# Performance work log

Measured on AMD Instinct MI355X. Metric: run time of the kernel, lower is better.

Reference implementation:

```python
import jax, jax.numpy as jnp
import numpy as np

B, T, C = 4, 2048, 1024
H = 16
D = C // H  # head_size = 64


def setup_inputs() -> dict:
    key = jax.random.key(0)
    k1, k2 = jax.random.split(key)
    x = jax.random.normal(k1, (B, T, C), dtype=jnp.float32)
    w_attn = jax.random.normal(k2, (C, 3 * C), dtype=jnp.float32) * (C ** -0.5)
    return {"x": x, "w_attn": w_attn}


def reference(x, w_attn):
    Bx, Tx, Cx = x.shape
    qkv = x @ w_attn                      # [B,T,3C] (no bias)
    q, k, v = jnp.split(qkv, 3, axis=-1)  # each [B,T,C]
    # [B,T,C] -> [B,H,T,D]
    q = q.reshape(Bx, Tx, H, D).transpose(0, 2, 1, 3)
    k = k.reshape(Bx, Tx, H, D).transpose(0, 2, 1, 3)
    v = v.reshape(Bx, Tx, H, D).transpose(0, 2, 1, 3)
    wei = jnp.einsum('bhqd,bhkd->bhqk', q, k) * (D ** -0.5)  # [B,H,T,T]
    causal = jnp.tril(jnp.ones((Tx, Tx), dtype=bool))
    wei = jnp.where(causal, wei, -jnp.inf)
    wei = jax.nn.softmax(wei, axis=-1)
    out = jnp.einsum('bhqk,bhkd->bhqd', wei, v)  # [B,H,T,D]
    out = out.transpose(0, 2, 1, 3).reshape(Bx, Tx, Cx)
    return out
```

## Files before the change

### kernel.cpp

```cpp
#include <hip/hip_runtime.h>
#include <hip/hip_bf16.h>

typedef __attribute__((ext_vector_type(8))) short bf16x8;
typedef __attribute__((ext_vector_type(4))) float f32x4;

#define T_SZ 2048
#define C_SZ 1024
#define H_SZ 16
#define D_SZ 64
#define N_SZ 3072
#define M_SZ 8192

__device__ __forceinline__ unsigned short f2bf(float f) {
    unsigned int u = __float_as_uint(f);
    unsigned int r = (u + 0x7fffu + ((u >> 16) & 1u)) >> 16;
    return (unsigned short)r;
}

__device__ __forceinline__ void gload_lds16(const void* g, void* l) {
    __builtin_amdgcn_global_load_lds(
        (const __attribute__((address_space(1))) unsigned int*)g,
        (__attribute__((address_space(3))) unsigned int*)l, 16, 0, 0);
}

__global__ __launch_bounds__(256) void k_convert(const float* __restrict__ in,
                                                 unsigned short* __restrict__ out, int n4) {
    int i = blockIdx.x * 256 + threadIdx.x;
    if (i >= n4) return;
    float4 v = ((const float4*)in)[i];
    ushort4 u;
    u.x = f2bf(v.x); u.y = f2bf(v.y); u.z = f2bf(v.z); u.w = f2bf(v.w);
    ((ushort4*)out)[i] = u;
}

__global__ __launch_bounds__(256) void k_transpose(const float* __restrict__ w,
                                                   unsigned short* __restrict__ wt) {
    __shared__ float tile[32][33];
    const int nb = blockIdx.x * 32;
    const int kb = blockIdx.y * 32;
    const int tx = threadIdx.x & 31;
    const int ty = threadIdx.x >> 5;
#pragma unroll
    for (int i = 0; i < 32; i += 8)
        tile[ty + i][tx] = w[(size_t)(kb + ty + i) * N_SZ + nb + tx];
    __syncthreads();
#pragma unroll
    for (int i = 0; i < 32; i += 8)
        wt[(size_t)(nb + ty + i) * C_SZ + kb + tx] = f2bf(tile[tx][ty + i]);
}

__global__ __launch_bounds__(256) void k_qkv_gemm(const unsigned short* __restrict__ A,
                                                  const unsigned short* __restrict__ Bt,
                                                  unsigned short* __restrict__ Qb,
                                                  unsigned short* __restrict__ Kb,
                                                  unsigned short* __restrict__ Vb) {
    __shared__ __align__(16) unsigned short As[128 * 32];
    __shared__ __align__(16) unsigned short Bs[128 * 32];
    const int tid = threadIdx.x;
    const int lane = tid & 63, wid = tid >> 6;
    const int wm = wid & 1, wn = wid >> 1;
    const int row0 = blockIdx.x * 128;
    const int col0 = blockIdx.y * 128;
    f32x4 acc[4][4] = {};
    const int c0 = 2 * wid, c1 = 2 * wid + 1;
    const int lr = lane >> 2, lk = (lane & 3) * 8;
    const int l15 = lane & 15, lg = lane >> 4;

    for (int kt = 0; kt < 1024; kt += 32) {
        __syncthreads();
        gload_lds16(A + (size_t)(row0 + c0 * 16 + lr) * 1024 + kt + lk, As + c0 * 512);
        gload_lds16(A + (size_t)(row0 + c1 * 16 + lr) * 1024 + kt + lk, As + c1 * 512);
        gload_lds16(Bt + (size_t)(col0 + c0 * 16 + lr) * 1024 + kt + lk, Bs + c0 * 512);
        gload_lds16(Bt + (size_t)(col0 + c1 * 16 + lr) * 1024 + kt + lk, Bs + c1 * 512);
        __syncthreads();
        bf16x8 af[4], bfr[4];
#pragma unroll
        for (int m = 0; m < 4; ++m)
            af[m] = *(const bf16x8*)&As[(wm * 64 + m * 16 + l15) * 32 + lg * 8];
#pragma unroll
        for (int n = 0; n < 4; ++n)
            bfr[n] = *(const bf16x8*)&Bs[(wn * 64 + n * 16 + l15) * 32 + lg * 8];
#pragma unroll
        for (int m = 0; m < 4; ++m)
#pragma unroll
            for (int n = 0; n < 4; ++n)
                acc[m][n] = __builtin_amdgcn_mfma_f32_16x16x32_bf16(af[m], bfr[n], acc[m][n], 0, 0, 0);
    }

    const int sel = col0 >> 10;
    unsigned short* dst = (sel == 0) ? Qb : ((sel == 1) ? Kb : Vb);
#pragma unroll
    for (int m = 0; m < 4; ++m) {
#pragma unroll
        for (int n = 0; n < 4; ++n) {
            int col = col0 + wn * 64 + n * 16 + l15;
            int cc = col & 1023;
            int h = cc >> 6, d = cc & 63;
#pragma unroll
            for (int i = 0; i < 4; ++i) {
                int row = row0 + wm * 64 + m * 16 + lg * 4 + i;
                int b = row >> 11, t = row & 2047;
                size_t idx = ((size_t)(b * 16 + h) * 2048 + t) * 64 + d;
                dst[idx] = f2bf(acc[m][n][i]);
            }
        }
    }
}

__global__ __launch_bounds__(256) void k_attn(const unsigned short* __restrict__ Qb,
                                              const unsigned short* __restrict__ Kb,
                                              const unsigned short* __restrict__ Vb,
                                              float* __restrict__ out) {
    const int qt = blockIdx.x;
    const int bh = blockIdx.y;
    const int bb = bh >> 4, hh = bh & 15;
    const unsigned short* Qp = Qb + (size_t)bh * T_SZ * D_SZ;
    const unsigned short* Kp = Kb + (size_t)bh * T_SZ * D_SZ;
    const unsigned short* Vp = Vb + (size_t)bh * T_SZ * D_SZ;
    const int tid = threadIdx.x, lane = tid & 63, wid = tid >> 6;
    const int l15 = lane & 15, lg = lane >> 4;
    const int q0 = qt * 64 + wid * 16;

    __shared__ __align__(16) unsigned short Vt[64][72];
    __shared__ __align__(16) unsigned short Pl[4][16][72];

    bf16x8 qf[2];
#pragma unroll
    for (int kh = 0; kh < 2; ++kh)
        qf[kh] = *(const bf16x8*)&Qp[(size_t)(q0 + l15) * 64 + kh * 32 + lg * 8];

    f32x4 oacc[4] = {};
    float mrow[4] = {-1e30f, -1e30f, -1e30f, -1e30f};
    float lrow[4] = {0.f, 0.f, 0.f, 0.f};
    const float scale = 0.125f;

    for (int kb = 0; kb <= qt; ++kb) {
        const int k0 = kb * 64;
        __syncthreads();
        {
            const int key = tid >> 2, dc = (tid & 3) * 16;
            bf16x8 v0 = *(const bf16x8*)&Vp[(size_t)(k0 + key) * 64 + dc];
            bf16x8 v1 = *(const bf16x8*)&Vp[(size_t)(k0 + key) * 64 + dc + 8];
#pragma unroll
            for (int j = 0; j < 8; ++j) {
                Vt[dc + j][key]     = (unsigned short)v0[j];
                Vt[dc + 8 + j][key] = (unsigned short)v1[j];
            }
        }
        __syncthreads();

        f32x4 s[4] = {};
#pragma unroll
        for (int ct = 0; ct < 4; ++ct) {
#pragma unroll
            for (int kh = 0; kh < 2; ++kh) {
                bf16x8 kf = *(const bf16x8*)&Kp[(size_t)(k0 + ct * 16 + l15) * 64 + kh * 32 + lg * 8];
                s[ct] = __builtin_amdgcn_mfma_f32_16x16x32_bf16(qf[kh], kf, s[ct], 0, 0, 0);
            }
        }
        if (kb == qt) {
#pragma unroll
            for (int ct = 0; ct < 4; ++ct) {
                int key = k0 + ct * 16 + l15;
#pragma unroll
                for (int i = 0; i < 4; ++i) {
                    int qrow = q0 + lg * 4 + i;
                    s[ct][i] = (key <= qrow) ? s[ct][i] * scale : -1e30f;
                }
            }
        } else {
#pragma unroll
            for (int ct = 0; ct < 4; ++ct)
#pragma unroll
                for (int i = 0; i < 4; ++i) s[ct][i] *= scale;
        }
        float p[4][4];
#pragma unroll
        for (int i = 0; i < 4; ++i) {
            float rmax = fmaxf(fmaxf(s[0][i], s[1][i]), fmaxf(s[2][i], s[3][i]));
            rmax = fmaxf(rmax, __shfl_xor(rmax, 1));
            rmax = fmaxf(rmax, __shfl_xor(rmax, 2));
            rmax = fmaxf(rmax, __shfl_xor(rmax, 4));
            rmax = fmaxf(rmax, __shfl_xor(rmax, 8));
            float mnew = fmaxf(mrow[i], rmax);
            float sc = __expf(mrow[i] - mnew);
            float rsum = 0.f;
#pragma unroll
            for (int ct = 0; ct < 4; ++ct) {
                float pv = __expf(s[ct][i] - mnew);
                p[ct][i] = pv;
                rsum += pv;
            }
            rsum += __shfl_xor(rsum, 1);
            rsum += __shfl_xor(rsum, 2);
            rsum += __shfl_xor(rsum, 4);
            rsum += __shfl_xor(rsum, 8);
            lrow[i] = lrow[i] * sc + rsum;
            mrow[i] = mnew;
#pragma unroll
            for (int ct = 0; ct < 4; ++ct) oacc[ct][i] *= sc;
        }
#pragma unroll
        for (int ct = 0; ct < 4; ++ct)
#pragma unroll
            for (int i = 0; i < 4; ++i)
                Pl[wid][lg * 4 + i][ct * 16 + l15] = f2bf(p[ct][i]);
#pragma unroll
        for (int ct = 0; ct < 4; ++ct) {
#pragma unroll
            for (int kh = 0; kh < 2; ++kh) {
                bf16x8 pf = *(const bf16x8*)&Pl[wid][l15][kh * 32 + lg * 8];
                bf16x8 vf = *(const bf16x8*)&Vt[ct * 16 + l15][kh * 32 + lg * 8];
                oacc[ct] = __builtin_amdgcn_mfma_f32_16x16x32_bf16(pf, vf, oacc[ct], 0, 0, 0);
            }
        }
    }
#pragma unroll
    for (int ct = 0; ct < 4; ++ct) {
#pragma unroll
        for (int i = 0; i < 4; ++i) {
            int qrow = q0 + lg * 4 + i;
            float val = oacc[ct][i] / lrow[i];
            out[((size_t)bb * T_SZ + qrow) * C_SZ + hh * 64 + ct * 16 + l15] = val;
        }
    }
}

extern "C" void kernel_launch(void* const* d_in, const int* in_sizes, int n_in,
                              void* d_out, int out_size, void* d_ws, size_t ws_size,
                              hipStream_t stream) {
    const float* x = (const float*)d_in[0];
    const float* w = (const float*)d_in[1];
    float* out = (float*)d_out;
    char* ws = (char*)d_ws;
    unsigned short* xb  = (unsigned short*)(ws);
    unsigned short* wtb = (unsigned short*)(ws + 16777216);
    unsigned short* Qb  = (unsigned short*)(ws + 16777216 + 6291456);
    unsigned short* Kb  = (unsigned short*)(ws + 16777216 + 6291456 + 16777216);
    unsigned short* Vb  = (unsigned short*)(ws + 16777216 + 6291456 + 2 * 16777216);

    k_convert<<<8192, 256, 0, stream>>>(x, xb, 2097152);
    k_transpose<<<dim3(96, 32), 256, 0, stream>>>(w, wtb);
    k_qkv_gemm<<<dim3(64, 24), 256, 0, stream>>>(xb, wtb, Qb, Kb, Vb);
    k_attn<<<dim3(32, 64), 256, 0, stream>>>(Qb, Kb, Vb, out);
}
```

Baseline: 388.0 us.

## Store V transposed from GEMM and restructure attention into 128-row register-fed blocks

The QKV GEMM epilogue now writes V in a transposed [b,h,d,t] layout using vectorised 4-element stores. The attention kernel therefore loads V fragments directly from global memory, removing the per-iteration LDS transpose and both block barriers. Each wave now handles two 16-row groups, so every query block covers 128 rows. K fragments are prefetched in registers for the next key tile, and the heaviest causal blocks are launched first. The cost is more register pressure and half as many blocks, which may lower occupancy.

```diff
diff --git a/kernel.cpp b/kernel.cpp
--- a/kernel.cpp
+++ b/kernel.cpp
@@ -53,7 +53,7 @@
                                                   const unsigned short* __restrict__ Bt,
                                                   unsigned short* __restrict__ Qb,
                                                   unsigned short* __restrict__ Kb,
-                                                  unsigned short* __restrict__ Vb) {
+                                                  unsigned short* __restrict__ Vtb) {
     __shared__ __align__(16) unsigned short As[128 * 32];
     __shared__ __align__(16) unsigned short Bs[128 * 32];
     const int tid = threadIdx.x;
@@ -88,141 +88,193 @@
     }
 
     const int sel = col0 >> 10;
-    unsigned short* dst = (sel == 0) ? Qb : ((sel == 1) ? Kb : Vb);
-#pragma unroll
-    for (int m = 0; m < 4; ++m) {
-#pragma unroll
-        for (int n = 0; n < 4; ++n) {
-            int col = col0 + wn * 64 + n * 16 + l15;
-            int cc = col & 1023;
-            int h = cc >> 6, d = cc & 63;
-#pragma unroll
-            for (int i = 0; i < 4; ++i) {
-                int row = row0 + wm * 64 + m * 16 + lg * 4 + i;
+    if (sel < 2) {
+        unsigned short* dst = (sel == 0) ? Qb : Kb;
+#pragma unroll
+        for (int m = 0; m < 4; ++m) {
+#pragma unroll
+            for (int n = 0; n < 4; ++n) {
+                int col = col0 + wn * 64 + n * 16 + l15;
+                int cc = col & 1023;
+                int h = cc >> 6, d = cc & 63;
+#pragma unroll
+                for (int i = 0; i < 4; ++i) {
+                    int row = row0 + wm * 64 + m * 16 + lg * 4 + i;
+                    int b = row >> 11, t = row & 2047;
+                    size_t idx = ((size_t)(b * 16 + h) * 2048 + t) * 64 + d;
+                    dst[idx] = f2bf(acc[m][n][i]);
+                }
+            }
+        }
+    } else {
+#pragma unroll
+        for (int m = 0; m < 4; ++m) {
+#pragma unroll
+            for (int n = 0; n < 4; ++n) {
+                int cc = (col0 + wn * 64 + n * 16 + l15) & 1023;
+                int h = cc >> 6, d = cc & 63;
+                int row = row0 + wm * 64 + m * 16 + lg * 4;
                 int b = row >> 11, t = row & 2047;
-                size_t idx = ((size_t)(b * 16 + h) * 2048 + t) * 64 + d;
-                dst[idx] = f2bf(acc[m][n][i]);
-            }
-        }
-    }
+                ushort4 u;
+                u.x = f2bf(acc[m][n][0]); u.y = f2bf(acc[m][n][1]);
+                u.z = f2bf(acc[m][n][2]); u.w = f2bf(acc[m][n][3]);
+                size_t idx = ((size_t)(b * 16 + h) * 64 + d) * 2048 + t;
+                *(ushort4*)&Vtb[idx] = u;
+            }
+        }
+    }
+}
+
+__device__ __forceinline__ void load_k(const unsigned short* __restrict__ Kp, int k0,
+                                       int l15, int lg, bf16x8 kf[4][2]) {
+#pragma unroll
+    for (int ct = 0; ct < 4; ++ct)
+#pragma unroll
+        for (int kh = 0; kh < 2; ++kh)
+            kf[ct][kh] = *(const bf16x8*)&Kp[(size_t)(k0 + ct * 16 + l15) * 64 + kh * 32 + lg * 8];
 }
 
 __global__ __launch_bounds__(256) void k_attn(const unsigned short* __restrict__ Qb,
                                               const unsigned short* __restrict__ Kb,
-                                              const unsigned short* __restrict__ Vb,
+                                              const unsigned short* __restrict__ Vt,
                                               float* __restrict__ out) {
-    const int qt = blockIdx.x;
+    const int qb = 15 - blockIdx.x;
     const int bh = blockIdx.y;
     const int bb = bh >> 4, hh = bh & 15;
     const unsigned short* Qp = Qb + (size_t)bh * T_SZ * D_SZ;
     const unsigned short* Kp = Kb + (size_t)bh * T_SZ * D_SZ;
-    const unsigned short* Vp = Vb + (size_t)bh * T_SZ * D_SZ;
+    const unsigned short* Vp = Vt + (size_t)bh * T_SZ * D_SZ;
     const int tid = threadIdx.x, lane = tid & 63, wid = tid >> 6;
     const int l15 = lane & 15, lg = lane >> 4;
-    const int q0 = qt * 64 + wid * 16;
-
-    __shared__ __align__(16) unsigned short Vt[64][72];
-    __shared__ __align__(16) unsigned short Pl[4][16][72];
-
-    bf16x8 qf[2];
-#pragma unroll
-    for (int kh = 0; kh < 2; ++kh)
-        qf[kh] = *(const bf16x8*)&Qp[(size_t)(q0 + l15) * 64 + kh * 32 + lg * 8];
-
-    f32x4 oacc[4] = {};
-    float mrow[4] = {-1e30f, -1e30f, -1e30f, -1e30f};
-    float lrow[4] = {0.f, 0.f, 0.f, 0.f};
+    const int rga0 = qb * 128 + wid * 32;
+
+    __shared__ __align__(16) unsigned short Pl[4][2][16][72];
+
+    bf16x8 qf[2][2];
+#pragma unroll
+    for (int rg = 0; rg < 2; ++rg)
+#pragma unroll
+        for (int kh = 0; kh < 2; ++kh)
+            qf[rg][kh] = *(const bf16x8*)&Qp[(size_t)(rga0 + rg * 16 + l15) * 64 + kh * 32 + lg * 8];
+
+    f32x4 oacc[2][4] = {};
+    float mrow[2][4], lrow[2][4];
+#pragma unroll
+    for (int rg = 0; rg < 2; ++rg)
+#pragma unroll
+        for (int i = 0; i < 4; ++i) { mrow[rg][i] = -1e30f; lrow[rg][i] = 0.f; }
+
+    const int kb_max = 2 * qb + 1;
     const float scale = 0.125f;
 
-    for (int kb = 0; kb <= qt; ++kb) {
+    bf16x8 kf[4][2];
+    load_k(Kp, 0, l15, lg, kf);
+
+    for (int kb = 0; kb <= kb_max; ++kb) {
         const int k0 = kb * 64;
-        __syncthreads();
-        {
-            const int key = tid >> 2, dc = (tid & 3) * 16;
-            bf16x8 v0 = *(const bf16x8*)&Vp[(size_t)(k0 + key) * 64 + dc];
-            bf16x8 v1 = *(const bf16x8*)&Vp[(size_t)(k0 + key) * 64 + dc + 8];
-#pragma unroll
-            for (int j = 0; j < 8; ++j) {
-                Vt[dc + j][key]     = (unsigned short)v0[j];
-                Vt[dc + 8 + j][key] = (unsigned short)v1[j];
-            }
-        }
-        __syncthreads();
-
-        f32x4 s[4] = {};
-#pragma unroll
-        for (int ct = 0; ct < 4; ++ct) {
-#pragma unroll
-            for (int kh = 0; kh < 2; ++kh) {
-                bf16x8 kf = *(const bf16x8*)&Kp[(size_t)(k0 + ct * 16 + l15) * 64 + kh * 32 + lg * 8];
-                s[ct] = __builtin_amdgcn_mfma_f32_16x16x32_bf16(qf[kh], kf, s[ct], 0, 0, 0);
-            }
-        }
-        if (kb == qt) {
+        bool act[2];
+        f32x4 s[2][4];
+#pragma unroll
+        for (int rg = 0; rg < 2; ++rg) {
+            const int rga = rga0 + rg * 16;
+            act[rg] = (k0 <= rga + 15);
+            if (!act[rg]) continue;
 #pragma unroll
             for (int ct = 0; ct < 4; ++ct) {
-                int key = k0 + ct * 16 + l15;
-#pragma unroll
-                for (int i = 0; i < 4; ++i) {
-                    int qrow = q0 + lg * 4 + i;
-                    s[ct][i] = (key <= qrow) ? s[ct][i] * scale : -1e30f;
-                }
-            }
-        } else {
+                f32x4 a = {};
+#pragma unroll
+                for (int kh = 0; kh < 2; ++kh)
+                    a = __builtin_amdgcn_mfma_f32_16x16x32_bf16(qf[rg][kh], kf[ct][kh], a, 0, 0, 0);
+                s[rg][ct] = a;
+            }
+        }
+        bf16x8 vf[4][2];
+#pragma unroll
+        for (int ct = 0; ct < 4; ++ct)
+#pragma unroll
+            for (int kh = 0; kh < 2; ++kh)
+                vf[ct][kh] = *(const bf16x8*)&Vp[(size_t)(ct * 16 + l15) * 2048 + k0 + kh * 32 + lg * 8];
+        if (kb < kb_max) load_k(Kp, k0 + 64, l15, lg, kf);
+
+#pragma unroll
+        for (int rg = 0; rg < 2; ++rg) {
+            if (!act[rg]) continue;
+            const int rga = rga0 + rg * 16;
+            if (k0 + 63 > rga) {
+#pragma unroll
+                for (int ct = 0; ct < 4; ++ct) {
+                    const int key = k0 + ct * 16 + l15;
+#pragma unroll
+                    for (int i = 0; i < 4; ++i) {
+                        const int qrow = rga + lg * 4 + i;
+                        s[rg][ct][i] = (key <= qrow) ? s[rg][ct][i] * scale : -1e30f;
+                    }
+                }
+            } else {
+#pragma unroll
+                for (int ct = 0; ct < 4; ++ct)
+#pragma unroll
+                    for (int i = 0; i < 4; ++i) s[rg][ct][i] *= scale;
+            }
+#pragma unroll
+            for (int i = 0; i < 4; ++i) {
+                float rmax = fmaxf(fmaxf(s[rg][0][i], s[rg][1][i]), fmaxf(s[rg][2][i], s[rg][3][i]));
+                rmax = fmaxf(rmax, __shfl_xor(rmax, 1));
+                rmax = fmaxf(rmax, __shfl_xor(rmax, 2));
+                rmax = fmaxf(rmax, __shfl_xor(rmax, 4));
+                rmax = fmaxf(rmax, __shfl_xor(rmax, 8));
+                float mnew = fmaxf(mrow[rg][i], rmax);
+                float sc = __expf(mrow[rg][i] - mnew);
+                float rsum = 0.f;
+#pragma unroll
+                for (int ct = 0; ct < 4; ++ct) {
+                    float pv = __expf(s[rg][ct][i] - mnew);
+                    s[rg][ct][i] = pv;
+                    rsum += pv;
+                }
+                rsum += __shfl_xor(rsum, 1);
+                rsum += __shfl_xor(rsum, 2);
+                rsum += __shfl_xor(rsum, 4);
+                rsum += __shfl_xor(rsum, 8);
+                lrow[rg][i] = lrow[rg][i] * sc + rsum;
+                mrow[rg][i] = mnew;
+#pragma unroll
+                for (int ct = 0; ct < 4; ++ct) oacc[rg][ct][i] *= sc;
+            }
 #pragma unroll
             for (int ct = 0; ct < 4; ++ct)
 #pragma unroll
-                for (int i = 0; i < 4; ++i) s[ct][i] *= scale;
-        }
-        float p[4][4];
-#pragma unroll
-        for (int i = 0; i < 4; ++i) {
-            float rmax = fmaxf(fmaxf(s[0][i], s[1][i]), fmaxf(s[2][i], s[3][i]));
-            rmax = fmaxf(rmax, __shfl_xor(rmax, 1));
-            rmax = fmaxf(rmax, __shfl_xor(rmax, 2));
-            rmax = fmaxf(rmax, __shfl_xor(rmax, 4));
-            rmax = fmaxf(rmax, __shfl_xor(rmax, 8));
-            float mnew = fmaxf(mrow[i], rmax);
-            float sc = __expf(mrow[i] - mnew);
-            float rsum = 0.f;
-#pragma unroll
-            for (int ct = 0; ct < 4; ++ct) {
-                float pv = __expf(s[ct][i] - mnew);
-                p[ct][i] = pv;
-                rsum += pv;
-            }
-            rsum += __shfl_xor(rsum, 1);
-            rsum += __shfl_xor(rsum, 2);
-            rsum += __shfl_xor(rsum, 4);
-            rsum += __shfl_xor(rsum, 8);
-            lrow[i] = lrow[i] * sc + rsum;
-            mrow[i] = mnew;
-#pragma unroll
-            for (int ct = 0; ct < 4; ++ct) oacc[ct][i] *= sc;
-        }
+                for (int i = 0; i < 4; ++i)
+                    Pl[wid][rg][lg * 4 + i][ct * 16 + l15] = f2bf(s[rg][ct][i]);
+        }
+
+#pragma unroll
+        for (int kh = 0; kh < 2; ++kh) {
+            bf16x8 pf[2];
+#pragma unroll
+            for (int rg = 0; rg < 2; ++rg)
+                if (act[rg]) pf[rg] = *(const bf16x8*)&Pl[wid][rg][l15][kh * 32 + lg * 8];
+#pragma unroll
+            for (int ct = 0; ct < 4; ++ct)
+#pragma unroll
+                for (int rg = 0; rg < 2; ++rg) {
+                    if (!act[rg]) continue;
+                    oacc[rg][ct] = __builtin_amdgcn_mfma_f32_16x16x32_bf16(pf[rg], vf[ct][kh], oacc[rg][ct], 0, 0, 0);
+                }
+        }
+    }
+
+#pragma unroll
+    for (int rg = 0; rg < 2; ++rg) {
+        const int rga = rga0 + rg * 16;
 #pragma unroll
         for (int ct = 0; ct < 4; ++ct)
 #pragma unroll
-            for (int i = 0; i < 4; ++i)
-                Pl[wid][lg * 4 + i][ct * 16 + l15] = f2bf(p[ct][i]);
-#pragma unroll
-        for (int ct = 0; ct < 4; ++ct) {
-#pragma unroll
-            for (int kh = 0; kh < 2; ++kh) {
-                bf16x8 pf = *(const bf16x8*)&Pl[wid][l15][kh * 32 + lg * 8];
-                bf16x8 vf = *(const bf16x8*)&Vt[ct * 16 + l15][kh * 32 + lg * 8];
-                oacc[ct] = __builtin_amdgcn_mfma_f32_16x16x32_bf16(pf, vf, oacc[ct], 0, 0, 0);
-            }
-        }
-    }
-#pragma unroll
-    for (int ct = 0; ct < 4; ++ct) {
-#pragma unroll
-        for (int i = 0; i < 4; ++i) {
-            int qrow = q0 + lg * 4 + i;
-            float val = oacc[ct][i] / lrow[i];
-            out[((size_t)bb * T_SZ + qrow) * C_SZ + hh * 64 + ct * 16 + l15] = val;
-        }
+            for (int i = 0; i < 4; ++i) {
+                const int qrow = rga + lg * 4 + i;
+                out[((size_t)bb * T_SZ + qrow) * C_SZ + hh * 64 + ct * 16 + l15] =
+                    oacc[rg][ct][i] / lrow[rg][i];
+            }
     }
 }
 
@@ -237,10 +289,10 @@
     unsigned short* wtb = (unsigned short*)(ws + 16777216);
     unsigned short* Qb  = (unsigned short*)(ws + 16777216 + 6291456);
     unsigned short* Kb  = (unsigned short*)(ws + 16777216 + 6291456 + 16777216);
-    unsigned short* Vb  = (unsigned short*)(ws + 16777216 + 6291456 + 2 * 16777216);
+    unsigned short* Vtb = (unsigned short*)(ws + 16777216 + 6291456 + 2 * 16777216);
 
     k_convert<<<8192, 256, 0, stream>>>(x, xb, 2097152);
     k_transpose<<<dim3(96, 32), 256, 0, stream>>>(w, wtb);
-    k_qkv_gemm<<<dim3(64, 24), 256, 0, stream>>>(xb, wtb, Qb, Kb, Vb);
-    k_attn<<<dim3(32, 64), 256, 0, stream>>>(Qb, Kb, Vb, out);
-}
+    k_qkv_gemm<<<dim3(64, 24), 256, 0, stream>>>(xb, wtb, Qb, Kb, Vtb);
+    k_attn<<<dim3(16, 64), 256, 0, stream>>>(Qb, Kb, Vtb, out);
+}
```

Measured after the change: 497.7 us. +28.3%, slower.
